# Optimization experiments

Measured on AMD Instinct MI355X. Metric: run time of the kernel, lower is better.

## Reference

```python
import jax, jax.numpy as jnp
import numpy as np

GAMMA = 0.001

N_TEST, N_TRAIN, D, OUT = 8192, 8192, 512, 16

def setup_inputs() -> dict:
    key = jax.random.key(0)
    k1, k2, k3 = jax.random.split(key, 3)
    X = jax.random.normal(k1, (N_TEST, D), dtype=jnp.float32)
    train_X = jax.random.normal(k2, (N_TRAIN, D), dtype=jnp.float32)
    alpha = jax.random.normal(k3, (N_TRAIN, OUT), dtype=jnp.float32)
    return {"X": X, "train_X": train_X, "alpha": alpha}


def reference(X, train_X, alpha):
    # (same math as (x[:,None]-y[None])**2 summed over d, without the n*m*d blowup)
    x_sq = jnp.sum(X * X, axis=-1, keepdims=True)            # [n_test, 1]
    y_sq = jnp.sum(train_X * train_X, axis=-1)[None, :]       # [1, n_train]
    cross = X @ train_X.T                                     # [n_test, n_train]
    sq = x_sq + y_sq - 2.0 * cross
    K_test = jnp.exp(-GAMMA * sq)
    return K_test @ alpha                                     # [n_test, out]
```

## Files before the change

kernel.cpp:

```cpp
#include <hip/hip_runtime.h>
#include <stdint.h>

#define NROW 8192
#define DIM  512
#define NOUT 16
#define GAMMA 0.001f
#define EXP2S (2.0f * GAMMA * 1.44269504088896340736f)
#define SC1 0x7F7F7F7F

typedef __bf16 bf16_t;
typedef bf16_t bf16x4_t __attribute__((ext_vector_type(4)));
typedef bf16_t bf16x8_t __attribute__((ext_vector_type(8)));
typedef float  floatx4_t __attribute__((ext_vector_type(4)));
typedef int    intx4_t  __attribute__((ext_vector_type(4)));
typedef int    intx8_t  __attribute__((ext_vector_type(8)));

__device__ __forceinline__ void async_copy16(const void* g, const void* l) {
    __builtin_amdgcn_global_load_lds(
        (__attribute__((address_space(1))) void*)(uintptr_t)g,
        (__attribute__((address_space(3))) void*)(uint32_t)(uintptr_t)l,
        16, 0, 0);
}

__global__ __launch_bounds__(256) void prep_convert(
    const float* __restrict__ X, const float* __restrict__ T,
    const float* __restrict__ alpha,
    uint8_t* __restrict__ Xf, uint8_t* __restrict__ Tf,
    float* __restrict__ xfac, bf16_t* __restrict__ alphaTp)
{
    const int w = threadIdx.x >> 6, lane = threadIdx.x & 63;
    const int row = blockIdx.x * 4 + w;
    const bool is_test = row < NROW;
    const float* src = is_test ? X : T;
    uint8_t* dst = is_test ? Xf : Tf;
    const int r = is_test ? row : row - NROW;
    const float4* s4 = (const float4*)(src + (size_t)r * DIM);
    const float4 v0 = s4[lane * 2];
    const float4 v1 = s4[lane * 2 + 1];
    float ss = v0.x*v0.x + v0.y*v0.y + v0.z*v0.z + v0.w*v0.w
             + v1.x*v1.x + v1.y*v1.y + v1.z*v1.z + v1.w*v1.w;
    int lo = __builtin_amdgcn_cvt_pk_fp8_f32(v0.x, v0.y, 0, false);
    lo     = __builtin_amdgcn_cvt_pk_fp8_f32(v0.z, v0.w, lo, true);
    int hi = __builtin_amdgcn_cvt_pk_fp8_f32(v1.x, v1.y, 0, false);
    hi     = __builtin_amdgcn_cvt_pk_fp8_f32(v1.z, v1.w, hi, true);
    *(int2*)(dst + (size_t)r * DIM + lane * 8) = make_int2(lo, hi);
#pragma unroll
    for (int m = 32; m > 0; m >>= 1) ss += __shfl_xor(ss, m, 64);
    const float f = __expf(-GAMMA * ss);
    if (is_test) {
        if (lane == 0) xfac[r] = f;
    } else if (lane < 16) {
        alphaTp[(size_t)lane * NROW + r] = (bf16_t)(alpha[r * 16 + lane] * f);
    }
}

#define TPT 4
#define KLD2 72

__global__ __launch_bounds__(512)
__attribute__((amdgpu_waves_per_eu(2, 2)))
void rbf_main(
    const uint8_t* __restrict__ Xf, const uint8_t* __restrict__ Tf,
    const bf16_t* __restrict__ alphaTp, const float* __restrict__ xfac,
    float* __restrict__ out)
{
    __shared__ __align__(16) unsigned char smem[36864];

    const int tid = threadIdx.x;
    const int w = tid >> 6, lane = tid & 63;
    const int wm = w >> 2, wn = w & 3;
    const int quad = lane >> 4, l15 = lane & 15;

    const int rb = blockIdx.x;
    const int chunk = blockIdx.y;
    const int row0 = rb * 128;
    const int cb0 = chunk * (TPT * 128);

    const int s_row = tid >> 3;
    const int s_ub = (((tid & 7) ^ (s_row & 7)) * 16);
    const uint8_t* gTp = Tf + (size_t)(cb0 + s_row) * DIM + s_ub;
    const unsigned ldsW = (unsigned)(w << 10);

    const int sw = l15 & 7;

    intx8_t xg[4][2];
#pragma unroll
    for (int g = 0; g < 4; ++g)
#pragma unroll
        for (int i = 0; i < 2; ++i)
            xg[g][i] = *(const intx8_t*)(Xf
                + (size_t)(row0 + wn * 32 + i * 16 + l15) * DIM
                + g * 128 + quad * 32);
#pragma unroll
    for (int g = 0; g < 4; ++g)
#pragma unroll
        for (int i = 0; i < 2; ++i)
            asm volatile("" : "+v"(xg[g][i]));

    const floatx4_t vzero = {0.f, 0.f, 0.f, 0.f};
    floatx4_t oacc[2];
#pragma unroll
    for (int i = 0; i < 2; ++i) oacc[i] = vzero;

    bf16_t* kw = (bf16_t*)smem + w * (32 * KLD2);

    for (int t = 0; t < TPT; ++t) {
        const uint8_t* gTt = gTp + (size_t)t * 128 * DIM;

        floatx4_t acc[4][2];
#pragma unroll
        for (int i = 0; i < 4; ++i)
#pragma unroll
            for (int j = 0; j < 2; ++j) acc[i][j] = vzero;

        __syncthreads();
#pragma unroll
        for (int i = 0; i < 2; ++i)
            async_copy16(gTt + (size_t)i * 32768, smem + i * 8192 + ldsW);

#pragma unroll
        for (int g = 0; g < 4; ++g) {
            __syncthreads();
            if (g < 3) {
                const unsigned bb = ((g + 1) & 1) * 16384u;
                const int kb = (g + 1) * 128;
#pragma unroll
                for (int i = 0; i < 2; ++i)
                    async_copy16(gTt + (size_t)i * 32768 + kb,
                                 smem + bb + i * 8192 + ldsW);
            }
            const unsigned char* bufc = smem + (g & 1) * 16384;
#pragma unroll
            for (int mi = 0; mi < 4; ++mi) {
                const int rA = wm * 64 + mi * 16 + l15;
                const intx4_t alo = *(const intx4_t*)(bufc + rA * 128 + (((2 * quad) ^ sw) * 16));
                const intx4_t ahi = *(const intx4_t*)(bufc + rA * 128 + (((2 * quad + 1) ^ sw) * 16));
                const intx8_t ta = __builtin_shufflevector(alo, ahi, 0, 1, 2, 3, 4, 5, 6, 7);
#pragma unroll
                for (int ni = 0; ni < 2; ++ni)
                    acc[mi][ni] = __builtin_amdgcn_mfma_scale_f32_16x16x128_f8f6f4(
                        ta, xg[g][ni], acc[mi][ni], 0, 0, 0, SC1, 0, SC1);
            }
        }

        __syncthreads();
#pragma unroll
        for (int ni = 0; ni < 2; ++ni)
#pragma unroll
            for (int mi = 0; mi < 4; ++mi) {
                bf16x4_t pk;
#pragma unroll
                for (int r = 0; r < 4; ++r)
                    pk[r] = (bf16_t)__builtin_amdgcn_exp2f(acc[mi][ni][r] * EXP2S);
                *(bf16x4_t*)(kw + (ni * 16 + l15) * KLD2 + mi * 16 + quad * 4) = pk;
            }

        const int cb = cb0 + t * 128;
#pragma unroll
        for (int ks = 0; ks < 2; ++ks) {
            const bf16x8_t bv = *(const bf16x8_t*)(alphaTp + (size_t)l15 * NROW
                                                   + cb + wm * 64 + ks * 32 + quad * 8);
#pragma unroll
            for (int ni = 0; ni < 2; ++ni) {
                const bf16x8_t av = *(const bf16x8_t*)(kw + (ni * 16 + l15) * KLD2
                                                       + ks * 32 + quad * 8);
                oacc[ni] = __builtin_amdgcn_mfma_f32_16x16x32_bf16(av, bv, oacc[ni], 0, 0, 0);
            }
        }
    }

    __syncthreads();
    float* stash = (float*)smem;
    if (wm == 1) {
#pragma unroll
        for (int ni = 0; ni < 2; ++ni)
            *(floatx4_t*)(stash + (wn * 2 + ni) * 256 + lane * 4) = oacc[ni];
    }
    __syncthreads();
    if (wm == 0) {
#pragma unroll
        for (int ni = 0; ni < 2; ++ni) {
            const floatx4_t o2 = *(const floatx4_t*)(stash + (wn * 2 + ni) * 256 + lane * 4);
            const int trow = row0 + wn * 32 + ni * 16 + quad * 4;
            const float4 xf = *(const float4*)(xfac + trow);
            atomicAdd(out + (size_t)(trow + 0) * NOUT + l15, (oacc[ni][0] + o2[0]) * xf.x);
            atomicAdd(out + (size_t)(trow + 1) * NOUT + l15, (oacc[ni][1] + o2[1]) * xf.y);
            atomicAdd(out + (size_t)(trow + 2) * NOUT + l15, (oacc[ni][2] + o2[2]) * xf.z);
            atomicAdd(out + (size_t)(trow + 3) * NOUT + l15, (oacc[ni][3] + o2[3]) * xf.w);
        }
    }
}

extern "C" void kernel_launch(void* const* d_in, const int* in_sizes, int n_in,
                              void* d_out, int out_size, void* d_ws, size_t ws_size,
                              hipStream_t stream) {
    (void)in_sizes; (void)n_in; (void)out_size; (void)ws_size;
    const float* X     = (const float*)d_in[0];
    const float* T     = (const float*)d_in[1];
    const float* alpha = (const float*)d_in[2];

    char* ws = (char*)d_ws;
    uint8_t* Xf     = (uint8_t*)ws;
    uint8_t* Tf     = (uint8_t*)(ws + (8u << 20));
    float*   xfac   = (float*)(ws + (16u << 20));
    bf16_t*  alphaTp= (bf16_t*)(ws + (16u << 20) + (64u << 10));
    float*   out    = (float*)d_out;

    hipMemsetAsync(out, 0, (size_t)NROW * NOUT * sizeof(float), stream);
    prep_convert<<<4096, 256, 0, stream>>>(X, T, alpha, Xf, Tf, xfac, alphaTp);
    dim3 grid(64, 16);
    rbf_main<<<grid, 512, 0, stream>>>(Xf, Tf, alphaTp, xfac, out);
}
```

Measured before the change: 143.6 us.

## Pre-tile fp8 operands into MFMA fragment order and prefetch next tile

After: 130.8 us. -9.0%, faster.

```diff
diff --git a/kernel.cpp b/kernel.cpp
--- a/kernel.cpp
+++ b/kernel.cpp
@@ -26,13 +26,16 @@
     const float* __restrict__ X, const float* __restrict__ T,
     const float* __restrict__ alpha,
     uint8_t* __restrict__ Xf, uint8_t* __restrict__ Tf,
-    float* __restrict__ xfac, bf16_t* __restrict__ alphaTp)
+    float* __restrict__ xfac, bf16_t* __restrict__ alphaTp,
+    float* __restrict__ out)
 {
+    const int zidx = blockIdx.x * 256 + threadIdx.x;
+    if (zidx < NROW * NOUT) out[zidx] = 0.f;
+
     const int w = threadIdx.x >> 6, lane = threadIdx.x & 63;
     const int row = blockIdx.x * 4 + w;
     const bool is_test = row < NROW;
     const float* src = is_test ? X : T;
-    uint8_t* dst = is_test ? Xf : Tf;
     const int r = is_test ? row : row - NROW;
     const float4* s4 = (const float4*)(src + (size_t)r * DIM);
     const float4 v0 = s4[lane * 2];
@@ -43,7 +46,17 @@
     lo     = __builtin_amdgcn_cvt_pk_fp8_f32(v0.z, v0.w, lo, true);
     int hi = __builtin_amdgcn_cvt_pk_fp8_f32(v1.x, v1.y, 0, false);
     hi     = __builtin_amdgcn_cvt_pk_fp8_f32(v1.z, v1.w, hi, true);
-    *(int2*)(dst + (size_t)r * DIM + lane * 8) = make_int2(lo, hi);
+    size_t off;
+    if (is_test) {
+        off = (size_t)(r >> 4) * 8192 + ((lane >> 4) * 2048)
+            + (((lane >> 2) & 3) * 512) + ((r & 15) * 32) + ((lane & 3) * 8);
+        *(int2*)(Xf + off) = make_int2(lo, hi);
+    } else {
+        off = (size_t)(r >> 4) * 8192 + ((lane >> 4) * 2048)
+            + (((lane >> 1) & 1) * 1024) + (((lane >> 2) & 3) * 256)
+            + ((r & 15) * 16) + ((lane & 1) * 8);
+        *(int2*)(Tf + off) = make_int2(lo, hi);
+    }
 #pragma unroll
     for (int m = 32; m > 0; m >>= 1) ss += __shfl_xor(ss, m, 64);
     const float f = __expf(-GAMMA * ss);
@@ -58,13 +71,13 @@
 #define KLD2 72
 
 __global__ __launch_bounds__(512)
-__attribute__((amdgpu_waves_per_eu(2, 2)))
+__attribute__((amdgpu_waves_per_eu(2, 4)))
 void rbf_main(
     const uint8_t* __restrict__ Xf, const uint8_t* __restrict__ Tf,
     const bf16_t* __restrict__ alphaTp, const float* __restrict__ xfac,
     float* __restrict__ out)
 {
-    __shared__ __align__(16) unsigned char smem[36864];
+    __shared__ __align__(16) unsigned char smem[69632];
 
     const int tid = threadIdx.x;
     const int w = tid >> 6, lane = tid & 63;
@@ -76,65 +89,60 @@
     const int row0 = rb * 128;
     const int cb0 = chunk * (TPT * 128);
 
-    const int s_row = tid >> 3;
-    const int s_ub = (((tid & 7) ^ (s_row & 7)) * 16);
-    const uint8_t* gTp = Tf + (size_t)(cb0 + s_row) * DIM + s_ub;
-    const unsigned ldsW = (unsigned)(w << 10);
-
-    const int sw = l15 & 7;
-
+    const uint8_t* xbase = Xf + (size_t)((row0 >> 4) + wn * 2) * 8192
+                              + quad * 512 + l15 * 32;
     intx8_t xg[4][2];
 #pragma unroll
     for (int g = 0; g < 4; ++g)
 #pragma unroll
         for (int i = 0; i < 2; ++i)
-            xg[g][i] = *(const intx8_t*)(Xf
-                + (size_t)(row0 + wn * 32 + i * 16 + l15) * DIM
-                + g * 128 + quad * 32);
+            xg[g][i] = *(const intx8_t*)(xbase + (size_t)i * 8192 + g * 2048);
 #pragma unroll
     for (int g = 0; g < 4; ++g)
 #pragma unroll
         for (int i = 0; i < 2; ++i)
             asm volatile("" : "+v"(xg[g][i]));
 
+    const uint8_t* gT0 = Tf + (size_t)((cb0 >> 4) + w) * 8192 + lane * 16;
+    const unsigned ldsT = (unsigned)(w * 2048);
+
     const floatx4_t vzero = {0.f, 0.f, 0.f, 0.f};
     floatx4_t oacc[2];
 #pragma unroll
     for (int i = 0; i < 2; ++i) oacc[i] = vzero;
 
-    bf16_t* kw = (bf16_t*)smem + w * (32 * KLD2);
-
+    bf16_t* kw = (bf16_t*)(smem + 32768 + w * 4608);
+
+#pragma unroll
+    for (int j1 = 0; j1 < 2; ++j1)
+        async_copy16(gT0 + j1 * 1024, smem + ldsT + j1 * 1024);
+
+#pragma unroll 1
     for (int t = 0; t < TPT; ++t) {
-        const uint8_t* gTt = gTp + (size_t)t * 128 * DIM;
-
         floatx4_t acc[4][2];
 #pragma unroll
         for (int i = 0; i < 4; ++i)
 #pragma unroll
             for (int j = 0; j < 2; ++j) acc[i][j] = vzero;
-
-        __syncthreads();
-#pragma unroll
-        for (int i = 0; i < 2; ++i)
-            async_copy16(gTt + (size_t)i * 32768, smem + i * 8192 + ldsW);
 
 #pragma unroll
         for (int g = 0; g < 4; ++g) {
             __syncthreads();
             if (g < 3) {
                 const unsigned bb = ((g + 1) & 1) * 16384u;
-                const int kb = (g + 1) * 128;
-#pragma unroll
-                for (int i = 0; i < 2; ++i)
-                    async_copy16(gTt + (size_t)i * 32768 + kb,
-                                 smem + bb + i * 8192 + ldsW);
+                const size_t gofs = (size_t)t * 8 * 8192 + (g + 1) * 2048;
+#pragma unroll
+                for (int j1 = 0; j1 < 2; ++j1)
+                    async_copy16(gT0 + gofs + j1 * 1024,
+                                 smem + bb + ldsT + j1 * 1024);
             }
             const unsigned char* bufc = smem + (g & 1) * 16384;
 #pragma unroll
             for (int mi = 0; mi < 4; ++mi) {
-                const int rA = wm * 64 + mi * 16 + l15;
-                const intx4_t alo = *(const intx4_t*)(bufc + rA * 128 + (((2 * quad) ^ sw) * 16));
-                const intx4_t ahi = *(const intx4_t*)(bufc + rA * 128 + (((2 * quad + 1) ^ sw) * 16));
+                const unsigned char* sb = bufc + (wm * 4 + mi) * 2048
+                                        + quad * 256 + l15 * 16;
+                const intx4_t alo = *(const intx4_t*)(sb);
+                const intx4_t ahi = *(const intx4_t*)(sb + 1024);
                 const intx8_t ta = __builtin_shufflevector(alo, ahi, 0, 1, 2, 3, 4, 5, 6, 7);
 #pragma unroll
                 for (int ni = 0; ni < 2; ++ni)
@@ -143,7 +151,6 @@
             }
         }
 
-        __syncthreads();
 #pragma unroll
         for (int ni = 0; ni < 2; ++ni)
 #pragma unroll
@@ -166,6 +173,14 @@
                                                        + ks * 32 + quad * 8);
                 oacc[ni] = __builtin_amdgcn_mfma_f32_16x16x32_bf16(av, bv, oacc[ni], 0, 0, 0);
             }
+        }
+
+        if (t + 1 < TPT) {
+            const size_t gofs = (size_t)(t + 1) * 8 * 8192;
+#pragma unroll
+            for (int j1 = 0; j1 < 2; ++j1)
+                async_copy16(gT0 + gofs + j1 * 1024,
+                             smem + ldsT + j1 * 1024);
         }
     }
 
@@ -206,8 +221,7 @@
     bf16_t*  alphaTp= (bf16_t*)(ws + (16u << 20) + (64u << 10));
     float*   out    = (float*)d_out;
 
-    hipMemsetAsync(out, 0, (size_t)NROW * NOUT * sizeof(float), stream);
-    prep_convert<<<4096, 256, 0, stream>>>(X, T, alpha, Xf, Tf, xfac, alphaTp);
+    prep_convert<<<4096, 256, 0, stream>>>(X, T, alpha, Xf, Tf, xfac, alphaTp, out);
     dim3 grid(64, 16);
     rbf_main<<<grid, 512, 0, stream>>>(Xf, Tf, alphaTp, xfac, out);
 }
```
